# Optimization experiments

Hardware: AMD Instinct MI355X
Metric: run time of the kernel (lower is better)

## Reference

```python
import jax, jax.numpy as jnp
import numpy as np

B, LP, NC, D, E = 8, 1000, 64, 128, 320  # batch, protein len, compound atoms, hid dim, esm dim


def _linear_params(key, din, dout):
    k1, k2 = jax.random.split(key)
    lim = 1.0 / np.sqrt(din)
    W = jax.random.uniform(k1, (din, dout), minval=-lim, maxval=lim, dtype=jnp.float32)
    b = jax.random.uniform(k2, (dout,), minval=-lim, maxval=lim, dtype=jnp.float32)
    return W, b


def setup_inputs() -> dict:
    key = jax.random.key(0)
    ks = jax.random.split(key, 14)
    inp = {
        "protein_embedding": jax.random.normal(ks[0], (B, LP, E), dtype=jnp.float32),
        "protein_feat_x": jax.random.normal(ks[1], (B, LP, D), dtype=jnp.float32),
        "compound_feats": jax.random.normal(ks[2], (B, NC, D), dtype=jnp.float32),
    }
    layers = [("emb", E, D), ("wq", D, D), ("wk", D, D), ("wv", D, D), ("wo", D, D),
              ("jp", D, D), ("jc", D, D),
              ("c1", D, 1024), ("c2", 1024, 1024), ("c3", 1024, 256), ("c4", 256, 1)]
    for i, (name, din, dout) in enumerate(layers):
        W, b = _linear_params(ks[3 + i], din, dout)
        inp[name + "_w"] = W
        inp[name + "_b"] = b
    return inp


def reference(protein_embedding, protein_feat_x, compound_feats,
              emb_w, emb_b, wq_w, wq_b, wk_w, wk_b, wv_w, wv_b, wo_w, wo_b,
              jp_w, jp_b, jc_w, jc_b,
              c1_w, c1_b, c2_w, c2_b, c3_w, c3_b, c4_w, c4_b):
    # protein sequence embedding -> hid dim
    pe = protein_embedding @ emb_w + emb_b                      # [B, LP, D]
    # single-head cross attention: query = seq embedding, key/value = graph feats
    Q = pe @ wq_w + wq_b
    K = protein_feat_x @ wk_w + wk_b
    V = protein_feat_x @ wv_w + wv_b
    scale = jnp.sqrt(jnp.asarray(D, pe.dtype))                  # n_heads=1 -> head_dim=D
    attn = jax.nn.softmax(jnp.einsum('bqd,bkd->bqk', Q, K) / scale, axis=-1)
    protein_feats = jnp.einsum('bqk,bkd->bqd', attn, V) @ wo_w + wo_b  # [B, LP, D]

    # sigmoid bilinear joint attention over (protein residue, compound atom) pairs
    P = jax.nn.relu(protein_feats) @ jp_w + jp_b                # [B, LP, D]
    C = jax.nn.relu(compound_feats) @ jc_w + jc_b               # [B, NC, D]
    A = jax.nn.sigmoid(jnp.einsum('bid,bkd->bik', P, C))        # [B, LP, NC]
    A = A / jnp.sum(A, axis=(1, 2), keepdims=True)

    # tanh outer product (the costly 4D bikj intermediate) then weighted reduction
    cp = jnp.tanh(protein_feats[:, :, None, :] * compound_feats[:, None, :, :])  # [B, LP, NC, D]
    cp_embedding = jnp.einsum('bikd,bik->bd', cp, A)            # [B, D]

    # classifier MLP (dropout is eval-mode identity)
    h = jax.nn.relu(cp_embedding @ c1_w + c1_b)
    h = jax.nn.relu(h @ c2_w + c2_b)
    h = jax.nn.relu(h @ c3_w + c3_b)
    return h @ c4_w + c4_b                                      # [B, 1]
```

## Files before the change

### kernel.cpp

```cpp
#include <hip/hip_runtime.h>
#include <hip/hip_bf16.h>
#include <math.h>

#define LP 1000
#define NCMP 64

__device__ __forceinline__ float rcp_fast(float x) { return __builtin_amdgcn_rcpf(x); }

template<bool RELU_IN>
__device__ __forceinline__ void gemm_body(const float* X, const float* W, const float* __restrict__ bias,
                                          float* Y, int K, int rowbase)
{
    __shared__ __align__(16) float Ws[32][128];
    __shared__ __align__(16) float Xt[32][36];
    const int t  = threadIdx.x;
    const int r0 = (t >> 5) * 4;
    const int c0 = (t & 31) * 4;
    const int xr = t >> 3, xk = (t & 7) << 2;
    const int xrow = rowbase + xr;
    float4 xv = *(const float4*)(X + (long)xrow * K + xk);
    float4 wv[4];
    #pragma unroll
    for (int u = 0; u < 4; ++u) {
        int s = t + u * 256, r = s >> 5, cb = (s & 31) << 2;
        wv[u] = *(const float4*)(W + (long)r * 128 + cb);
    }
    float acc[4][4] = {};
    for (int k0 = 0; k0 < K; k0 += 32) {
        float4 xs = xv;
        if (RELU_IN) { xs.x = fmaxf(xs.x,0.f); xs.y = fmaxf(xs.y,0.f);
                       xs.z = fmaxf(xs.z,0.f); xs.w = fmaxf(xs.w,0.f); }
        Xt[xk+0][xr] = xs.x; Xt[xk+1][xr] = xs.y; Xt[xk+2][xr] = xs.z; Xt[xk+3][xr] = xs.w;
        #pragma unroll
        for (int u = 0; u < 4; ++u) {
            int s = t + u * 256, r = s >> 5, cb = (s & 31) << 2;
            *(float4*)&Ws[r][cb] = wv[u];
        }
        __syncthreads();
        if (k0 + 32 < K) {
            xv = *(const float4*)(X + (long)xrow * K + k0 + 32 + xk);
            #pragma unroll
            for (int u = 0; u < 4; ++u) {
                int s = t + u * 256, r = s >> 5, cb = (s & 31) << 2;
                wv[u] = *(const float4*)(W + (long)(k0 + 32 + r) * 128 + cb);
            }
        }
        #pragma unroll
        for (int kk = 0; kk < 32; ++kk) {
            float4 w4 = *(const float4*)&Ws[kk][c0];
            float4 x4 = *(const float4*)&Xt[kk][r0];
            acc[0][0] = fmaf(x4.x, w4.x, acc[0][0]); acc[0][1] = fmaf(x4.x, w4.y, acc[0][1]);
            acc[0][2] = fmaf(x4.x, w4.z, acc[0][2]); acc[0][3] = fmaf(x4.x, w4.w, acc[0][3]);
            acc[1][0] = fmaf(x4.y, w4.x, acc[1][0]); acc[1][1] = fmaf(x4.y, w4.y, acc[1][1]);
            acc[1][2] = fmaf(x4.y, w4.z, acc[1][2]); acc[1][3] = fmaf(x4.y, w4.w, acc[1][3]);
            acc[2][0] = fmaf(x4.z, w4.x, acc[2][0]); acc[2][1] = fmaf(x4.z, w4.y, acc[2][1]);
            acc[2][2] = fmaf(x4.z, w4.z, acc[2][2]); acc[2][3] = fmaf(x4.z, w4.w, acc[2][3]);
            acc[3][0] = fmaf(x4.w, w4.x, acc[3][0]); acc[3][1] = fmaf(x4.w, w4.y, acc[3][1]);
            acc[3][2] = fmaf(x4.w, w4.z, acc[3][2]); acc[3][3] = fmaf(x4.w, w4.w, acc[3][3]);
        }
        __syncthreads();
    }
    float4 bv = *(const float4*)(bias + c0);
    #pragma unroll
    for (int i = 0; i < 4; ++i) {
        int row = rowbase + r0 + i;
        float4 o;
        o.x = acc[i][0] + bv.x; o.y = acc[i][1] + bv.y;
        o.z = acc[i][2] + bv.z; o.w = acc[i][3] + bv.w;
        *(float4*)(Y + (long)row * 128 + c0) = o;
    }
}

__global__ __launch_bounds__(256) void pre0_k(const float* __restrict__ emb_w, const float* __restrict__ emb_b,
                                              const float* __restrict__ wq_w, const float* __restrict__ wq_b,
                                              const float* __restrict__ wv_w, const float* __restrict__ wv_b,
                                              const float* __restrict__ wo_w, const float* __restrict__ wo_b,
                                              const float* __restrict__ zeros,
                                              float* __restrict__ Wp, float* __restrict__ bp,
                                              float* __restrict__ Wvo, float* __restrict__ bvo)
{
    const int bid = blockIdx.x;
    if (bid < 10) { gemm_body<false>(emb_w, wq_w, zeros, Wp, 128, bid * 32); return; }
    if (bid >= 11 && bid < 15) { gemm_body<false>(wv_w, wo_w, zeros, Wvo, 128, (bid - 11) * 32); return; }
    int n = threadIdx.x;
    if (n < 128) {
        const float* vb = (bid == 10) ? emb_b : wv_b;
        const float* Wm = (bid == 10) ? wq_w  : wo_w;
        const float* ab = (bid == 10) ? wq_b  : wo_b;
        float a0 = 0.f, a1 = 0.f, a2 = 0.f, a3 = 0.f;
        for (int k = 0; k < 128; k += 4) {
            a0 = fmaf(vb[k+0], Wm[(k+0)*128 + n], a0);
            a1 = fmaf(vb[k+1], Wm[(k+1)*128 + n], a1);
            a2 = fmaf(vb[k+2], Wm[(k+2)*128 + n], a2);
            a3 = fmaf(vb[k+3], Wm[(k+3)*128 + n], a3);
        }
        float* dst = (bid == 10) ? bp : bvo;
        dst[n] = (a0 + a1) + (a2 + a3) + ab[n];
    }
}

__global__ __launch_bounds__(256) void qkv_k(const float* __restrict__ PE, const float* __restrict__ Wp,
                                             const float* __restrict__ bp, const float* __restrict__ PFX,
                                             const float* __restrict__ wk_w, const float* __restrict__ wk_b,
                                             const float* __restrict__ CF, const float* __restrict__ jc_w,
                                             const float* __restrict__ jc_b,
                                             float* __restrict__ Qo, float* __restrict__ Ko, float* __restrict__ Cj)
{
    if (blockIdx.x < 250)
        gemm_body<false>(PE, Wp, bp, Qo, 320, blockIdx.x * 32);
    else if (blockIdx.x < 500)
        gemm_body<false>(PFX, wk_w, wk_b, Ko, 128, (blockIdx.x - 250) * 32);
    else
        gemm_body<true>(CF, jc_w, jc_b, Cj, 128, (blockIdx.x - 500) * 32);
}

__global__ __launch_bounds__(256) void flash_k(const float* __restrict__ Q, const float* __restrict__ Kg,
                                               const float* __restrict__ Vg, float* __restrict__ Opart,
                                               float* __restrict__ mpart, float* __restrict__ lpart)
{
    __shared__ __align__(16) float Qs[32][132];
    __shared__ __align__(16) float KVs[64][132];
    __shared__ __align__(16) float Ps[32][68];
    const int t  = threadIdx.x;
    const int tr = t >> 4;
    const int tc = t & 15;
    const int qt = blockIdx.x, sp = blockIdx.y, b = blockIdx.z;
    const int q0 = qt * 32;
    const float SCALE = 0.08838834764831845f;
    const float L2E   = 1.4426950408889634f;

    #pragma unroll
    for (int u = 0; u < 4; ++u) {
        int s = t + u * 256;
        int r = s >> 5, cb = (s & 31) << 2;
        float4 v = make_float4(0.f, 0.f, 0.f, 0.f);
        if (q0 + r < LP) v = *(const float4*)(Q + ((long)b * LP + q0 + r) * 128 + cb);
        Qs[r][cb] = v.x; Qs[r][cb + 1] = v.y; Qs[r][cb + 2] = v.z; Qs[r][cb + 3] = v.w;
    }
    float m_i[2] = { -3.0e38f, -3.0e38f };
    float l_i[2] = { 0.f, 0.f };
    float Oa[2][8] = {};

    for (int kt = sp * 8; kt < sp * 8 + 8; ++kt) {
        const int key0 = kt * 64;
        __syncthreads();
        #pragma unroll
        for (int u = 0; u < 8; ++u) {
            int s = t + u * 256;
            int r = s >> 5, cb = (s & 31) << 2;
            float4 v = make_float4(0.f, 0.f, 0.f, 0.f);
            if (key0 + r < LP) v = *(const float4*)(Kg + ((long)b * LP + key0 + r) * 128 + cb);
            KVs[r][cb] = v.x; KVs[r][cb + 1] = v.y; KVs[r][cb + 2] = v.z; KVs[r][cb + 3] = v.w;
        }
        __syncthreads();
        float sacc[2][4] = {};
        #pragma unroll 4
        for (int d4 = 0; d4 < 32; ++d4) {
            float4 q0v = *(const float4*)&Qs[2 * tr][d4 << 2];
            float4 q1v = *(const float4*)&Qs[2 * tr + 1][d4 << 2];
            #pragma unroll
            for (int j = 0; j < 4; ++j) {
                float4 kv = *(const float4*)&KVs[tc + (j << 4)][d4 << 2];
                sacc[0][j] += q0v.x * kv.x + q0v.y * kv.y + q0v.z * kv.z + q0v.w * kv.w;
                sacc[1][j] += q1v.x * kv.x + q1v.y * kv.y + q1v.z * kv.z + q1v.w * kv.w;
            }
        }
        __syncthreads();
        float4 vreg[8];
        #pragma unroll
        for (int u = 0; u < 8; ++u) {
            int s = t + u * 256;
            int r = s >> 5, cb = (s & 31) << 2;
            float4 v = make_float4(0.f, 0.f, 0.f, 0.f);
            if (key0 + r < LP) v = *(const float4*)(Vg + ((long)b * LP + key0 + r) * 128 + cb);
            vreg[u] = v;
        }
        #pragma unroll
        for (int j = 0; j < 4; ++j) {
            bool valid = (key0 + tc + (j << 4)) < LP;
            #pragma unroll
            for (int i = 0; i < 2; ++i) {
                float sv = sacc[i][j] * SCALE;
                sacc[i][j] = valid ? sv : -3.0e38f;
            }
        }
        #pragma unroll
        for (int i = 0; i < 2; ++i) {
            float tm = fmaxf(fmaxf(sacc[i][0], sacc[i][1]), fmaxf(sacc[i][2], sacc[i][3]));
            tm = fmaxf(tm, __shfl_xor(tm, 1));
            tm = fmaxf(tm, __shfl_xor(tm, 2));
            tm = fmaxf(tm, __shfl_xor(tm, 4));
            tm = fmaxf(tm, __shfl_xor(tm, 8));
            float mnew  = fmaxf(m_i[i], tm);
            float alpha = exp2f((m_i[i] - mnew) * L2E);
            float ps = 0.f;
            #pragma unroll
            for (int j = 0; j < 4; ++j) {
                float p = exp2f((sacc[i][j] - mnew) * L2E);
                Ps[2 * tr + i][tc + (j << 4)] = p;
                ps += p;
            }
            ps += __shfl_xor(ps, 1);
            ps += __shfl_xor(ps, 2);
            ps += __shfl_xor(ps, 4);
            ps += __shfl_xor(ps, 8);
            l_i[i] = l_i[i] * alpha + ps;
            m_i[i] = mnew;
            #pragma unroll
            for (int j = 0; j < 8; ++j) Oa[i][j] *= alpha;
        }
        #pragma unroll
        for (int u = 0; u < 8; ++u) {
            int s = t + u * 256;
            int r = s >> 5, cb = (s & 31) << 2;
            KVs[r][cb] = vreg[u].x; KVs[r][cb + 1] = vreg[u].y;
            KVs[r][cb + 2] = vreg[u].z; KVs[r][cb + 3] = vreg[u].w;
        }
        __syncthreads();
        #pragma unroll 2
        for (int c = 0; c < 64; ++c) {
            float4 va = *(const float4*)&KVs[c][tc << 2];
            float4 vb = *(const float4*)&KVs[c][64 + (tc << 2)];
            float p0 = Ps[2 * tr][c];
            float p1 = Ps[2 * tr + 1][c];
            Oa[0][0] = fmaf(p0, va.x, Oa[0][0]); Oa[0][1] = fmaf(p0, va.y, Oa[0][1]);
            Oa[0][2] = fmaf(p0, va.z, Oa[0][2]); Oa[0][3] = fmaf(p0, va.w, Oa[0][3]);
            Oa[0][4] = fmaf(p0, vb.x, Oa[0][4]); Oa[0][5] = fmaf(p0, vb.y, Oa[0][5]);
            Oa[0][6] = fmaf(p0, vb.z, Oa[0][6]); Oa[0][7] = fmaf(p0, vb.w, Oa[0][7]);
            Oa[1][0] = fmaf(p1, va.x, Oa[1][0]); Oa[1][1] = fmaf(p1, va.y, Oa[1][1]);
            Oa[1][2] = fmaf(p1, va.z, Oa[1][2]); Oa[1][3] = fmaf(p1, va.w, Oa[1][3]);
            Oa[1][4] = fmaf(p1, vb.x, Oa[1][4]); Oa[1][5] = fmaf(p1, vb.y, Oa[1][5]);
            Oa[1][6] = fmaf(p1, vb.z, Oa[1][6]); Oa[1][7] = fmaf(p1, vb.w, Oa[1][7]);
        }
    }
    #pragma unroll
    for (int i = 0; i < 2; ++i) {
        int row = q0 + 2 * tr + i;
        if (row < LP) {
            long base = (((long)sp * 8 + b) * LP + row) * 128;
            *(float4*)(Opart + base + (tc << 2))      = make_float4(Oa[i][0], Oa[i][1], Oa[i][2], Oa[i][3]);
            *(float4*)(Opart + base + 64 + (tc << 2)) = make_float4(Oa[i][4], Oa[i][5], Oa[i][6], Oa[i][7]);
            if (tc == 0) {
                mpart[((long)sp * 8 + b) * LP + row] = m_i[i];
                lpart[((long)sp * 8 + b) * LP + row] = l_i[i];
            }
        }
    }
}

__global__ __launch_bounds__(256) void megatail_k(
    const float* __restrict__ Opart, const float* __restrict__ mp, const float* __restrict__ lp,
    const float* __restrict__ Wvo, const float* __restrict__ bvo,
    const float* __restrict__ jp_w, const float* __restrict__ jp_b,
    const float* __restrict__ Cj, const float* __restrict__ CF,
    float* __restrict__ Asum, float* __restrict__ cpe)
{
    __shared__ __align__(16) float WsA[32][132];
    __shared__ __align__(16) float Xt[32][20];
    __shared__ __align__(16) float AttS[16][132];
    __shared__ __align__(16) float Csh[64][132];
    __shared__ float Ash[16][64];
    __shared__ float red[256];
    const int t = threadIdx.x;
    const int p0 = blockIdx.x * 16;
    const int b  = blockIdx.y;
    const float L2E = 1.4426950408889634f;

    #pragma unroll
    for (int u = 0; u < 8; ++u) {
        int s = t + u * 256, r = s >> 5, cb = (s & 31) << 2;
        float4 v = *(const float4*)(Cj + ((long)b * NCMP + r) * 128 + cb);
        Csh[r][cb] = v.x; Csh[r][cb+1] = v.y; Csh[r][cb+2] = v.z; Csh[r][cb+3] = v.w;
    }

    const int r0 = (t >> 5) * 2, c0 = (t & 31) * 4;
    const int xr = t >> 3, xk = (t & 7) << 2;
    int prow = p0 + xr; if (prow > LP - 1) prow = LP - 1;
    const long g = (long)b * LP + prow;
    float w0 = 0.f, w1 = 0.f, linv = 0.f;
    if (t < 128) {
        float m0 = mp[g], m1 = mp[g + 8000];
        float l0 = lp[g], l1 = lp[g + 8000];
        float mm = fmaxf(m0, m1);
        w0 = exp2f((m0 - mm) * L2E); w1 = exp2f((m1 - mm) * L2E);
        linv = 1.0f / (w0 * l0 + w1 * l1);
    }
    float4 xv = make_float4(0.f,0.f,0.f,0.f);
    float4 wv[4];
    if (t < 128) {
        float4 a = *(const float4*)(Opart + g * 128 + xk);
        float4 c = *(const float4*)(Opart + 1024000 + g * 128 + xk);
        xv.x = (w0*a.x + w1*c.x) * linv; xv.y = (w0*a.y + w1*c.y) * linv;
        xv.z = (w0*a.z + w1*c.z) * linv; xv.w = (w0*a.w + w1*c.w) * linv;
    }
    #pragma unroll
    for (int u = 0; u < 4; ++u) {
        int s = t + u * 256, r = s >> 5, cb = (s & 31) << 2;
        wv[u] = *(const float4*)(Wvo + (long)r * 128 + cb);
    }
    float acc[2][4] = {};
    for (int k0 = 0; k0 < 128; k0 += 32) {
        if (t < 128) { Xt[xk+0][xr]=xv.x; Xt[xk+1][xr]=xv.y; Xt[xk+2][xr]=xv.z; Xt[xk+3][xr]=xv.w; }
        #pragma unroll
        for (int u = 0; u < 4; ++u) {
            int s = t + u * 256, r = s >> 5, cb = (s & 31) << 2;
            *(float4*)&WsA[r][cb] = wv[u];
        }
        __syncthreads();
        if (k0 + 32 < 128) {
            int kn = k0 + 32;
            if (t < 128) {
                float4 a = *(const float4*)(Opart + g * 128 + kn + xk);
                float4 c = *(const float4*)(Opart + 1024000 + g * 128 + kn + xk);
                xv.x = (w0*a.x + w1*c.x) * linv; xv.y = (w0*a.y + w1*c.y) * linv;
                xv.z = (w0*a.z + w1*c.z) * linv; xv.w = (w0*a.w + w1*c.w) * linv;
            }
            #pragma unroll
            for (int u = 0; u < 4; ++u) {
                int s = t + u * 256, r = s >> 5, cb = (s & 31) << 2;
                wv[u] = *(const float4*)(Wvo + (long)(kn + r) * 128 + cb);
            }
        }
        #pragma unroll
        for (int kk = 0; kk < 32; ++kk) {
            float2 x2 = *(const float2*)&Xt[kk][r0];
            float4 w4 = *(const float4*)&WsA[kk][c0];
            acc[0][0]=fmaf(x2.x,w4.x,acc[0][0]); acc[0][1]=fmaf(x2.x,w4.y,acc[0][1]);
            acc[0][2]=fmaf(x2.x,w4.z,acc[0][2]); acc[0][3]=fmaf(x2.x,w4.w,acc[0][3]);
            acc[1][0]=fmaf(x2.y,w4.x,acc[1][0]); acc[1][1]=fmaf(x2.y,w4.y,acc[1][1]);
            acc[1][2]=fmaf(x2.y,w4.z,acc[1][2]); acc[1][3]=fmaf(x2.y,w4.w,acc[1][3]);
        }
        __syncthreads();
    }
    {
        float4 bv1 = *(const float4*)(bvo + c0);
        #pragma unroll
        for (int i = 0; i < 2; ++i) {
            float4 o = make_float4(acc[i][0]+bv1.x, acc[i][1]+bv1.y, acc[i][2]+bv1.z, acc[i][3]+bv1.w);
            *(float4*)&AttS[r0 + i][c0] = o;
        }
    }
    float4 wv2[4];
    #pragma unroll
    for (int u = 0; u < 4; ++u) {
        int s = t + u * 256, r = s >> 5, cb = (s & 31) << 2;
        wv2[u] = *(const float4*)(jp_w + (long)r * 128 + cb);
    }
    float ac2[2][4] = {};
    for (int k0 = 0; k0 < 128; k0 += 32) {
        #pragma unroll
        for (int u = 0; u < 4; ++u) {
            int s = t + u * 256, r = s >> 5, cb = (s & 31) << 2;
            *(float4*)&WsA[r][cb] = wv2[u];
        }
        __syncthreads();
        if (k0 + 32 < 128) {
            #pragma unroll
            for (int u = 0; u < 4; ++u) {
                int s = t + u * 256, r = s >> 5, cb = (s & 31) << 2;
                wv2[u] = *(const float4*)(jp_w + (long)(k0 + 32 + r) * 128 + cb);
            }
        }
        #pragma unroll
        for (int kk = 0; kk < 32; ++kk) {
            float x0 = fmaxf(AttS[r0 + 0][k0 + kk], 0.f);
            float x1 = fmaxf(AttS[r0 + 1][k0 + kk], 0.f);
            float4 w4 = *(const float4*)&WsA[kk][c0];
            ac2[0][0]=fmaf(x0,w4.x,ac2[0][0]); ac2[0][1]=fmaf(x0,w4.y,ac2[0][1]);
            ac2[0][2]=fmaf(x0,w4.z,ac2[0][2]); ac2[0][3]=fmaf(x0,w4.w,ac2[0][3]);
            ac2[1][0]=fmaf(x1,w4.x,ac2[1][0]); ac2[1][1]=fmaf(x1,w4.y,ac2[1][1]);
            ac2[1][2]=fmaf(x1,w4.z,ac2[1][2]); ac2[1][3]=fmaf(x1,w4.w,ac2[1][3]);
        }
        __syncthreads();
    }
    float (*Psh)[132] = WsA;
    {
        float4 b2 = *(const float4*)(jp_b + c0);
        #pragma unroll
        for (int i = 0; i < 2; ++i)
            *(float4*)&Psh[r0 + i][c0] =
                make_float4(ac2[i][0]+b2.x, ac2[i][1]+b2.y, ac2[i][2]+b2.z, ac2[i][3]+b2.w);
    }
    __syncthreads();
    const int tr = t >> 4, tc = t & 15;
    float sacc[4] = {};
    #pragma unroll 4
    for (int d4 = 0; d4 < 32; ++d4) {
        float4 p4 = *(const float4*)&Psh[tr][d4 << 2];
        #pragma unroll
        for (int j = 0; j < 4; ++j) {
            float4 cv = *(const float4*)&Csh[tc + (j << 4)][d4 << 2];
            sacc[j] += p4.x*cv.x + p4.y*cv.y + p4.z*cv.z + p4.w*cv.w;
        }
    }
    float lsum = 0.f;
    {
        int gi = p0 + tr;
        #pragma unroll
        for (int j = 0; j < 4; ++j) {
            float sg = rcp_fast(1.f + exp2f(-sacc[j] * L2E));
            if (gi < LP) { Ash[tr][tc + (j << 4)] = sg; lsum += sg; }
        }
    }
    red[t] = lsum;
    __syncthreads();
    for (int off = 128; off > 0; off >>= 1) {
        if (t < off) red[t] += red[t + off];
        __syncthreads();
    }
    if (t == 0) atomicAdd(Asum + b, red[0]);
    __syncthreads();
    #pragma unroll
    for (int u = 0; u < 8; ++u) {
        int s = t + u * 256, r = s >> 5, cb = (s & 31) << 2;
        float4 v = *(const float4*)(CF + ((long)b * NCMP + r) * 128 + cb);
        Csh[r][cb] = v.x; Csh[r][cb+1] = v.y; Csh[r][cb+2] = v.z; Csh[r][cb+3] = v.w;
    }
    __syncthreads();
    const float TWO_L2E = 2.8853900817779268f;
    const int d  = t & 127;
    const int kh = t >> 7;
    const int iiN = (LP - p0 < 16) ? (LP - p0) : 16;
    float accD = 0.f;
    for (int ii = 0; ii < iiN; ++ii) {
        float ptl = AttS[ii][d] * TWO_L2E;
        #pragma unroll
        for (int kk = 0; kk < 32; ++kk) {
            int k = (kh << 5) + kk;
            float e  = exp2f(ptl * Csh[k][d]);
            float th = 1.f - 2.f * rcp_fast(e + 1.f);
            accD = fmaf(th, Ash[ii][k], accD);
        }
    }
    red[t] = accD;
    __syncthreads();
    if (t < 128) atomicAdd(cpe + (long)b * 128 + t, red[t] + red[t + 128]);
}

__global__ __launch_bounds__(256) void c1h_k(const float* __restrict__ cpe, const float* __restrict__ Asum,
                                             const float* __restrict__ W, const float* __restrict__ bias,
                                             float* __restrict__ h1)
{
    __shared__ float sc[8][128];
    const int t = threadIdx.x;
    #pragma unroll
    for (int u = 0; u < 4; ++u) {
        int idx = t + u * 256;
        sc[idx >> 7][idx & 127] = cpe[idx] * rcp_fast(Asum[idx >> 7]);
    }
    __syncthreads();
    const int b = t >> 5, n = blockIdx.x * 32 + (t & 31);
    float a0 = 0.f, a1 = 0.f, a2 = 0.f, a3 = 0.f;
    #pragma unroll 8
    for (int k = 0; k < 128; k += 4) {
        a0 = fmaf(sc[b][k+0], W[(long)(k+0)*1024 + n], a0);
        a1 = fmaf(sc[b][k+1], W[(long)(k+1)*1024 + n], a1);
        a2 = fmaf(sc[b][k+2], W[(long)(k+2)*1024 + n], a2);
        a3 = fmaf(sc[b][k+3], W[(long)(k+3)*1024 + n], a3);
    }
    h1[b * 1024 + n] = fmaxf((a0 + a1) + (a2 + a3) + bias[n], 0.f);
}

__global__ __launch_bounds__(256) void c2_part_k(const float* __restrict__ in, const float* __restrict__ W,
                                                 float* __restrict__ part)
{
    __shared__ float ins[8][16];
    const int t = threadIdx.x, ks = blockIdx.x, k0 = ks * 16;
    if (t < 128) {
        int b = t >> 4, kk = t & 15;
        ins[b][kk] = in[b * 1024 + k0 + kk];
    }
    __syncthreads();
    const int n = (t & 63) * 4 + (t >> 6) * 256;
    float4 acc[8] = {};
    #pragma unroll
    for (int kk = 0; kk < 16; ++kk) {
        float4 w4 = *(const float4*)(W + (long)(k0 + kk) * 1024 + n);
        #pragma unroll
        for (int b = 0; b < 8; ++b) {
            float s = ins[b][kk];
            acc[b].x = fmaf(s, w4.x, acc[b].x); acc[b].y = fmaf(s, w4.y, acc[b].y);
            acc[b].z = fmaf(s, w4.z, acc[b].z); acc[b].w = fmaf(s, w4.w, acc[b].w);
        }
    }
    #pragma unroll
    for (int b = 0; b < 8; ++b)
        *(float4*)(part + ((long)(ks * 8 + b)) * 1024 + n) = acc[b];
}

__global__ __launch_bounds__(256) void c3m_k(const float* __restrict__ part2, const float* __restrict__ c2_b,
                                             const float* __restrict__ c3_w, const float* __restrict__ c3_b,
                                             const float* __restrict__ c4_w, const float* __restrict__ c4_b,
                                             float* __restrict__ out)
{
    __shared__ float Hs[1024];
    __shared__ float red[256];
    const int t = threadIdx.x, b = blockIdx.x;
    float4 acc4 = make_float4(0.f,0.f,0.f,0.f);
    #pragma unroll 4
    for (int ks = 0; ks < 64; ++ks) {
        float4 p = *(const float4*)(part2 + ((long)(ks * 8 + b)) * 1024 + t * 4);
        acc4.x += p.x; acc4.y += p.y; acc4.z += p.z; acc4.w += p.w;
    }
    {
        float4 bb = *(const float4*)(c2_b + t * 4);
        Hs[t*4+0] = fmaxf(acc4.x + bb.x, 0.f);
        Hs[t*4+1] = fmaxf(acc4.y + bb.y, 0.f);
        Hs[t*4+2] = fmaxf(acc4.z + bb.z, 0.f);
        Hs[t*4+3] = fmaxf(acc4.w + bb.w, 0.f);
    }
    __syncthreads();
    float a0 = 0.f, a1 = 0.f, a2 = 0.f, a3 = 0.f;
    #pragma unroll 8
    for (int k = 0; k < 1024; k += 4) {
        a0 = fmaf(Hs[k+0], c3_w[(long)(k+0)*256 + t], a0);
        a1 = fmaf(Hs[k+1], c3_w[(long)(k+1)*256 + t], a1);
        a2 = fmaf(Hs[k+2], c3_w[(long)(k+2)*256 + t], a2);
        a3 = fmaf(Hs[k+3], c3_w[(long)(k+3)*256 + t], a3);
    }
    float h3v = fmaxf((a0 + a1) + (a2 + a3) + c3_b[t], 0.f);
    red[t] = h3v * c4_w[t];
    __syncthreads();
    for (int off = 128; off > 0; off >>= 1) {
        if (t < off) red[t] += red[t + off];
        __syncthreads();
    }
    if (t == 0) out[b] = red[0] + c4_b[0];
}

extern "C" void kernel_launch(void* const* d_in, const int* in_sizes, int n_in,
                              void* d_out, int out_size, void* d_ws, size_t ws_size,
                              hipStream_t stream)
{
    const float* PE   = (const float*)d_in[0];
    const float* PFX  = (const float*)d_in[1];
    const float* CF   = (const float*)d_in[2];
    const float* emb_w = (const float*)d_in[3];  const float* emb_b = (const float*)d_in[4];
    const float* wq_w  = (const float*)d_in[5];  const float* wq_b  = (const float*)d_in[6];
    const float* wk_w  = (const float*)d_in[7];  const float* wk_b  = (const float*)d_in[8];
    const float* wv_w  = (const float*)d_in[9];  const float* wv_b  = (const float*)d_in[10];
    const float* wo_w  = (const float*)d_in[11]; const float* wo_b  = (const float*)d_in[12];
    const float* jp_w  = (const float*)d_in[13]; const float* jp_b  = (const float*)d_in[14];
    const float* jc_w  = (const float*)d_in[15]; const float* jc_b  = (const float*)d_in[16];
    const float* c1_w  = (const float*)d_in[17]; const float* c1_b  = (const float*)d_in[18];
    const float* c2_w  = (const float*)d_in[19]; const float* c2_b  = (const float*)d_in[20];
    const float* c3_w  = (const float*)d_in[21]; const float* c3_b  = (const float*)d_in[22];
    const float* c4_w  = (const float*)d_in[23]; const float* c4_b  = (const float*)d_in[24];

    float* ws     = (float*)d_ws;
    float* bufQ   = ws;
    float* bufK   = bufQ   + 1024000;
    float* bufC   = bufK   + 1024000;
    float* Opart  = bufC   + 65536;
    float* mpart  = Opart  + 2048000;
    float* lpart  = mpart  + 16000;
    float* Asum   = lpart  + 16000;
    float* cpe    = Asum   + 8;
    float* zeros  = cpe    + 1024;
    float* bprime = zeros  + 128;
    float* bufWp  = bprime + 128;
    float* bufWvo = bufWp  + 40960;
    float* bufbvo = bufWvo + 16384;
    float* h1     = bufbvo + 128;
    float* part2  = bufQ;

    hipMemsetAsync(Asum, 0, (8 + 1024 + 128) * sizeof(float), stream);

    pre0_k<<<16, 256, 0, stream>>>(emb_w, emb_b, wq_w, wq_b, wv_w, wv_b, wo_w, wo_b,
                                   zeros, bufWp, bprime, bufWvo, bufbvo);
    qkv_k<<<516, 256, 0, stream>>>(PE, bufWp, bprime, PFX, wk_w, wk_b, CF, jc_w, jc_b,
                                   bufQ, bufK, bufC);
    flash_k<<<dim3(32, 2, 8), 256, 0, stream>>>(bufQ, bufK, PFX, Opart, mpart, lpart);
    megatail_k<<<dim3(63, 8), 256, 0, stream>>>(Opart, mpart, lpart, bufWvo, bufbvo,
                                                jp_w, jp_b, bufC, CF, Asum, cpe);
    c1h_k<<<32, 256, 0, stream>>>(cpe, Asum, c1_w, c1_b, h1);
    c2_part_k<<<64, 256, 0, stream>>>(h1, c2_w, part2);
    c3m_k<<<8, 256, 0, stream>>>(part2, c2_b, c3_w, c3_b, c4_w, c4_b, (float*)d_out);
}
```

Before: 336.4 us.

## Retile flash attention to 48-row tiles with three-way key split; fuse c1 into c2

The flash attention kernel now gives each thread three query rows instead of two (48-row tiles) and splits the key range three ways instead of two, giving 504 blocks instead of 512 with more register reuse of each K/V load. The P·V loop reads probabilities as float4. The merge in the tail kernel is generalized to NSPLIT partials. The c1 layer is fused into the c2 partial kernel, which removes a launch and the h1 buffer. In exchange, each c12 block recomputes a small c1 slice, and register pressure in the attention kernel goes up.

```diff
diff --git a/kernel.cpp b/kernel.cpp
--- a/kernel.cpp
+++ b/kernel.cpp
@@ -4,6 +4,7 @@
 
 #define LP 1000
 #define NCMP 64
+#define NSPLIT 3
 
 __device__ __forceinline__ float rcp_fast(float x) { return __builtin_amdgcn_rcpf(x); }
 
@@ -114,78 +115,78 @@
         gemm_body<true>(CF, jc_w, jc_b, Cj, 128, (blockIdx.x - 500) * 32);
 }
 
-__global__ __launch_bounds__(256) void flash_k(const float* __restrict__ Q, const float* __restrict__ Kg,
-                                               const float* __restrict__ Vg, float* __restrict__ Opart,
-                                               float* __restrict__ mpart, float* __restrict__ lpart)
-{
-    __shared__ __align__(16) float Qs[32][132];
+__global__ __launch_bounds__(256) void flash6_k(const float* __restrict__ Q, const float* __restrict__ Kg,
+                                                const float* __restrict__ Vg, float* __restrict__ Opart,
+                                                float* __restrict__ mpart, float* __restrict__ lpart)
+{
+    __shared__ __align__(16) float Qs[48][132];
     __shared__ __align__(16) float KVs[64][132];
-    __shared__ __align__(16) float Ps[32][68];
+    __shared__ __align__(16) float Ps[48][68];
     const int t  = threadIdx.x;
     const int tr = t >> 4;
     const int tc = t & 15;
     const int qt = blockIdx.x, sp = blockIdx.y, b = blockIdx.z;
-    const int q0 = qt * 32;
+    const int q0 = qt * 48;
+    const int kt0 = (sp * 16) / NSPLIT;
+    const int kt1 = ((sp + 1) * 16) / NSPLIT;
     const float SCALE = 0.08838834764831845f;
     const float L2E   = 1.4426950408889634f;
 
     #pragma unroll
-    for (int u = 0; u < 4; ++u) {
-        int s = t + u * 256;
-        int r = s >> 5, cb = (s & 31) << 2;
+    for (int u = 0; u < 6; ++u) {
+        int s = t + u * 256, r = s >> 5, cb = (s & 31) << 2;
         float4 v = make_float4(0.f, 0.f, 0.f, 0.f);
         if (q0 + r < LP) v = *(const float4*)(Q + ((long)b * LP + q0 + r) * 128 + cb);
-        Qs[r][cb] = v.x; Qs[r][cb + 1] = v.y; Qs[r][cb + 2] = v.z; Qs[r][cb + 3] = v.w;
-    }
-    float m_i[2] = { -3.0e38f, -3.0e38f };
-    float l_i[2] = { 0.f, 0.f };
-    float Oa[2][8] = {};
-
-    for (int kt = sp * 8; kt < sp * 8 + 8; ++kt) {
+        *(float4*)&Qs[r][cb] = v;
+    }
+    float m_i[3] = { -3.0e38f, -3.0e38f, -3.0e38f };
+    float l_i[3] = { 0.f, 0.f, 0.f };
+    float Oa[3][8] = {};
+
+    for (int kt = kt0; kt < kt1; ++kt) {
         const int key0 = kt * 64;
         __syncthreads();
         #pragma unroll
         for (int u = 0; u < 8; ++u) {
-            int s = t + u * 256;
-            int r = s >> 5, cb = (s & 31) << 2;
+            int s = t + u * 256, r = s >> 5, cb = (s & 31) << 2;
             float4 v = make_float4(0.f, 0.f, 0.f, 0.f);
             if (key0 + r < LP) v = *(const float4*)(Kg + ((long)b * LP + key0 + r) * 128 + cb);
-            KVs[r][cb] = v.x; KVs[r][cb + 1] = v.y; KVs[r][cb + 2] = v.z; KVs[r][cb + 3] = v.w;
-        }
-        __syncthreads();
-        float sacc[2][4] = {};
+            *(float4*)&KVs[r][cb] = v;
+        }
+        __syncthreads();
+        float sacc[3][4] = {};
         #pragma unroll 4
         for (int d4 = 0; d4 < 32; ++d4) {
-            float4 q0v = *(const float4*)&Qs[2 * tr][d4 << 2];
-            float4 q1v = *(const float4*)&Qs[2 * tr + 1][d4 << 2];
+            float4 q0v = *(const float4*)&Qs[3 * tr + 0][d4 << 2];
+            float4 q1v = *(const float4*)&Qs[3 * tr + 1][d4 << 2];
+            float4 q2v = *(const float4*)&Qs[3 * tr + 2][d4 << 2];
             #pragma unroll
             for (int j = 0; j < 4; ++j) {
                 float4 kv = *(const float4*)&KVs[tc + (j << 4)][d4 << 2];
-                sacc[0][j] += q0v.x * kv.x + q0v.y * kv.y + q0v.z * kv.z + q0v.w * kv.w;
-                sacc[1][j] += q1v.x * kv.x + q1v.y * kv.y + q1v.z * kv.z + q1v.w * kv.w;
+                sacc[0][j] += q0v.x*kv.x + q0v.y*kv.y + q0v.z*kv.z + q0v.w*kv.w;
+                sacc[1][j] += q1v.x*kv.x + q1v.y*kv.y + q1v.z*kv.z + q1v.w*kv.w;
+                sacc[2][j] += q2v.x*kv.x + q2v.y*kv.y + q2v.z*kv.z + q2v.w*kv.w;
             }
         }
         __syncthreads();
         float4 vreg[8];
         #pragma unroll
         for (int u = 0; u < 8; ++u) {
-            int s = t + u * 256;
-            int r = s >> 5, cb = (s & 31) << 2;
-            float4 v = make_float4(0.f, 0.f, 0.f, 0.f);
-            if (key0 + r < LP) v = *(const float4*)(Vg + ((long)b * LP + key0 + r) * 128 + cb);
-            vreg[u] = v;
+            int s = t + u * 256, r = s >> 5, cb = (s & 31) << 2;
+            vreg[u] = make_float4(0.f, 0.f, 0.f, 0.f);
+            if (key0 + r < LP) vreg[u] = *(const float4*)(Vg + ((long)b * LP + key0 + r) * 128 + cb);
         }
         #pragma unroll
         for (int j = 0; j < 4; ++j) {
             bool valid = (key0 + tc + (j << 4)) < LP;
             #pragma unroll
-            for (int i = 0; i < 2; ++i) {
+            for (int i = 0; i < 3; ++i) {
                 float sv = sacc[i][j] * SCALE;
                 sacc[i][j] = valid ? sv : -3.0e38f;
             }
         }
         #pragma unroll
-        for (int i = 0; i < 2; ++i) {
+        for (int i = 0; i < 3; ++i) {
             float tm = fmaxf(fmaxf(sacc[i][0], sacc[i][1]), fmaxf(sacc[i][2], sacc[i][3]));
             tm = fmaxf(tm, __shfl_xor(tm, 1));
             tm = fmaxf(tm, __shfl_xor(tm, 2));
@@ -197,7 +198,7 @@
             #pragma unroll
             for (int j = 0; j < 4; ++j) {
                 float p = exp2f((sacc[i][j] - mnew) * L2E);
-                Ps[2 * tr + i][tc + (j << 4)] = p;
+                Ps[3 * tr + i][tc + (j << 4)] = p;
                 ps += p;
             }
             ps += __shfl_xor(ps, 1);
@@ -211,38 +212,48 @@
         }
         #pragma unroll
         for (int u = 0; u < 8; ++u) {
-            int s = t + u * 256;
-            int r = s >> 5, cb = (s & 31) << 2;
-            KVs[r][cb] = vreg[u].x; KVs[r][cb + 1] = vreg[u].y;
-            KVs[r][cb + 2] = vreg[u].z; KVs[r][cb + 3] = vreg[u].w;
+            int s = t + u * 256, r = s >> 5, cb = (s & 31) << 2;
+            *(float4*)&KVs[r][cb] = vreg[u];
         }
         __syncthreads();
         #pragma unroll 2
-        for (int c = 0; c < 64; ++c) {
-            float4 va = *(const float4*)&KVs[c][tc << 2];
-            float4 vb = *(const float4*)&KVs[c][64 + (tc << 2)];
-            float p0 = Ps[2 * tr][c];
-            float p1 = Ps[2 * tr + 1][c];
-            Oa[0][0] = fmaf(p0, va.x, Oa[0][0]); Oa[0][1] = fmaf(p0, va.y, Oa[0][1]);
-            Oa[0][2] = fmaf(p0, va.z, Oa[0][2]); Oa[0][3] = fmaf(p0, va.w, Oa[0][3]);
-            Oa[0][4] = fmaf(p0, vb.x, Oa[0][4]); Oa[0][5] = fmaf(p0, vb.y, Oa[0][5]);
-            Oa[0][6] = fmaf(p0, vb.z, Oa[0][6]); Oa[0][7] = fmaf(p0, vb.w, Oa[0][7]);
-            Oa[1][0] = fmaf(p1, va.x, Oa[1][0]); Oa[1][1] = fmaf(p1, va.y, Oa[1][1]);
-            Oa[1][2] = fmaf(p1, va.z, Oa[1][2]); Oa[1][3] = fmaf(p1, va.w, Oa[1][3]);
-            Oa[1][4] = fmaf(p1, vb.x, Oa[1][4]); Oa[1][5] = fmaf(p1, vb.y, Oa[1][5]);
-            Oa[1][6] = fmaf(p1, vb.z, Oa[1][6]); Oa[1][7] = fmaf(p1, vb.w, Oa[1][7]);
-        }
-    }
-    #pragma unroll
-    for (int i = 0; i < 2; ++i) {
-        int row = q0 + 2 * tr + i;
+        for (int cg = 0; cg < 16; ++cg) {
+            float4 pa = *(const float4*)&Ps[3 * tr + 0][cg << 2];
+            float4 pb = *(const float4*)&Ps[3 * tr + 1][cg << 2];
+            float4 pc = *(const float4*)&Ps[3 * tr + 2][cg << 2];
+            #pragma unroll
+            for (int e = 0; e < 4; ++e) {
+                int c = (cg << 2) + e;
+                float4 va = *(const float4*)&KVs[c][tc << 2];
+                float4 vb = *(const float4*)&KVs[c][64 + (tc << 2)];
+                float p0 = (e == 0) ? pa.x : (e == 1) ? pa.y : (e == 2) ? pa.z : pa.w;
+                float p1 = (e == 0) ? pb.x : (e == 1) ? pb.y : (e == 2) ? pb.z : pb.w;
+                float p2 = (e == 0) ? pc.x : (e == 1) ? pc.y : (e == 2) ? pc.z : pc.w;
+                Oa[0][0] = fmaf(p0, va.x, Oa[0][0]); Oa[0][1] = fmaf(p0, va.y, Oa[0][1]);
+                Oa[0][2] = fmaf(p0, va.z, Oa[0][2]); Oa[0][3] = fmaf(p0, va.w, Oa[0][3]);
+                Oa[0][4] = fmaf(p0, vb.x, Oa[0][4]); Oa[0][5] = fmaf(p0, vb.y, Oa[0][5]);
+                Oa[0][6] = fmaf(p0, vb.z, Oa[0][6]); Oa[0][7] = fmaf(p0, vb.w, Oa[0][7]);
+                Oa[1][0] = fmaf(p1, va.x, Oa[1][0]); Oa[1][1] = fmaf(p1, va.y, Oa[1][1]);
+                Oa[1][2] = fmaf(p1, va.z, Oa[1][2]); Oa[1][3] = fmaf(p1, va.w, Oa[1][3]);
+                Oa[1][4] = fmaf(p1, vb.x, Oa[1][4]); Oa[1][5] = fmaf(p1, vb.y, Oa[1][5]);
+                Oa[1][6] = fmaf(p1, vb.z, Oa[1][6]); Oa[1][7] = fmaf(p1, vb.w, Oa[1][7]);
+                Oa[2][0] = fmaf(p2, va.x, Oa[2][0]); Oa[2][1] = fmaf(p2, va.y, Oa[2][1]);
+                Oa[2][2] = fmaf(p2, va.z, Oa[2][2]); Oa[2][3] = fmaf(p2, va.w, Oa[2][3]);
+                Oa[2][4] = fmaf(p2, vb.x, Oa[2][4]); Oa[2][5] = fmaf(p2, vb.y, Oa[2][5]);
+                Oa[2][6] = fmaf(p2, vb.z, Oa[2][6]); Oa[2][7] = fmaf(p2, vb.w, Oa[2][7]);
+            }
+        }
+    }
+    #pragma unroll
+    for (int i = 0; i < 3; ++i) {
+        int row = q0 + 3 * tr + i;
         if (row < LP) {
-            long base = (((long)sp * 8 + b) * LP + row) * 128;
+            long base = ((long)sp * 1024000) + ((long)b * LP + row) * 128;
             *(float4*)(Opart + base + (tc << 2))      = make_float4(Oa[i][0], Oa[i][1], Oa[i][2], Oa[i][3]);
             *(float4*)(Opart + base + 64 + (tc << 2)) = make_float4(Oa[i][4], Oa[i][5], Oa[i][6], Oa[i][7]);
             if (tc == 0) {
-                mpart[((long)sp * 8 + b) * LP + row] = m_i[i];
-                lpart[((long)sp * 8 + b) * LP + row] = l_i[i];
+                mpart[(long)sp * 8000 + b * LP + row] = m_i[i];
+                lpart[(long)sp * 8000 + b * LP + row] = l_i[i];
             }
         }
     }
@@ -269,29 +280,37 @@
     #pragma unroll
     for (int u = 0; u < 8; ++u) {
         int s = t + u * 256, r = s >> 5, cb = (s & 31) << 2;
-        float4 v = *(const float4*)(Cj + ((long)b * NCMP + r) * 128 + cb);
-        Csh[r][cb] = v.x; Csh[r][cb+1] = v.y; Csh[r][cb+2] = v.z; Csh[r][cb+3] = v.w;
+        *(float4*)&Csh[r][cb] = *(const float4*)(Cj + ((long)b * NCMP + r) * 128 + cb);
     }
 
     const int r0 = (t >> 5) * 2, c0 = (t & 31) * 4;
     const int xr = t >> 3, xk = (t & 7) << 2;
     int prow = p0 + xr; if (prow > LP - 1) prow = LP - 1;
     const long g = (long)b * LP + prow;
-    float w0 = 0.f, w1 = 0.f, linv = 0.f;
+    float wgt[NSPLIT]; float linv = 0.f;
     if (t < 128) {
-        float m0 = mp[g], m1 = mp[g + 8000];
-        float l0 = lp[g], l1 = lp[g + 8000];
-        float mm = fmaxf(m0, m1);
-        w0 = exp2f((m0 - mm) * L2E); w1 = exp2f((m1 - mm) * L2E);
-        linv = 1.0f / (w0 * l0 + w1 * l1);
+        float mm = -3.0e38f;
+        #pragma unroll
+        for (int s = 0; s < NSPLIT; ++s) mm = fmaxf(mm, mp[g + (long)s * 8000]);
+        float ls = 0.f;
+        #pragma unroll
+        for (int s = 0; s < NSPLIT; ++s) {
+            wgt[s] = exp2f((mp[g + (long)s * 8000] - mm) * L2E);
+            ls += wgt[s] * lp[g + (long)s * 8000];
+        }
+        linv = 1.0f / ls;
     }
     float4 xv = make_float4(0.f,0.f,0.f,0.f);
     float4 wv[4];
     if (t < 128) {
-        float4 a = *(const float4*)(Opart + g * 128 + xk);
-        float4 c = *(const float4*)(Opart + 1024000 + g * 128 + xk);
-        xv.x = (w0*a.x + w1*c.x) * linv; xv.y = (w0*a.y + w1*c.y) * linv;
-        xv.z = (w0*a.z + w1*c.z) * linv; xv.w = (w0*a.w + w1*c.w) * linv;
+        float4 a = make_float4(0.f,0.f,0.f,0.f);
+        #pragma unroll
+        for (int s = 0; s < NSPLIT; ++s) {
+            float4 p = *(const float4*)(Opart + (long)s * 1024000 + g * 128 + xk);
+            a.x = fmaf(wgt[s], p.x, a.x); a.y = fmaf(wgt[s], p.y, a.y);
+            a.z = fmaf(wgt[s], p.z, a.z); a.w = fmaf(wgt[s], p.w, a.w);
+        }
+        xv = make_float4(a.x * linv, a.y * linv, a.z * linv, a.w * linv);
     }
     #pragma unroll
     for (int u = 0; u < 4; ++u) {
@@ -310,10 +329,14 @@
         if (k0 + 32 < 128) {
             int kn = k0 + 32;
             if (t < 128) {
-                float4 a = *(const float4*)(Opart + g * 128 + kn + xk);
-                float4 c = *(const float4*)(Opart + 1024000 + g * 128 + kn + xk);
-                xv.x = (w0*a.x + w1*c.x) * linv; xv.y = (w0*a.y + w1*c.y) * linv;
-                xv.z = (w0*a.z + w1*c.z) * linv; xv.w = (w0*a.w + w1*c.w) * linv;
+                float4 a = make_float4(0.f,0.f,0.f,0.f);
+                #pragma unroll
+                for (int s = 0; s < NSPLIT; ++s) {
+                    float4 p = *(const float4*)(Opart + (long)s * 1024000 + g * 128 + kn + xk);
+                    a.x = fmaf(wgt[s], p.x, a.x); a.y = fmaf(wgt[s], p.y, a.y);
+                    a.z = fmaf(wgt[s], p.z, a.z); a.w = fmaf(wgt[s], p.w, a.w);
+                }
+                xv = make_float4(a.x * linv, a.y * linv, a.z * linv, a.w * linv);
             }
             #pragma unroll
             for (int u = 0; u < 4; ++u) {
@@ -335,10 +358,9 @@
     {
         float4 bv1 = *(const float4*)(bvo + c0);
         #pragma unroll
-        for (int i = 0; i < 2; ++i) {
-            float4 o = make_float4(acc[i][0]+bv1.x, acc[i][1]+bv1.y, acc[i][2]+bv1.z, acc[i][3]+bv1.w);
-            *(float4*)&AttS[r0 + i][c0] = o;
-        }
+        for (int i = 0; i < 2; ++i)
+            *(float4*)&AttS[r0 + i][c0] =
+                make_float4(acc[i][0]+bv1.x, acc[i][1]+bv1.y, acc[i][2]+bv1.z, acc[i][3]+bv1.w);
     }
     float4 wv2[4];
     #pragma unroll
@@ -413,8 +435,7 @@
     #pragma unroll
     for (int u = 0; u < 8; ++u) {
         int s = t + u * 256, r = s >> 5, cb = (s & 31) << 2;
-        float4 v = *(const float4*)(CF + ((long)b * NCMP + r) * 128 + cb);
-        Csh[r][cb] = v.x; Csh[r][cb+1] = v.y; Csh[r][cb+2] = v.z; Csh[r][cb+3] = v.w;
+        *(float4*)&Csh[r][cb] = *(const float4*)(CF + ((long)b * NCMP + r) * 128 + cb);
     }
     __syncthreads();
     const float TWO_L2E = 2.8853900817779268f;
@@ -437,45 +458,38 @@
     if (t < 128) atomicAdd(cpe + (long)b * 128 + t, red[t] + red[t + 128]);
 }
 
-__global__ __launch_bounds__(256) void c1h_k(const float* __restrict__ cpe, const float* __restrict__ Asum,
-                                             const float* __restrict__ W, const float* __restrict__ bias,
-                                             float* __restrict__ h1)
+__global__ __launch_bounds__(256) void c12_k(const float* __restrict__ cpe, const float* __restrict__ Asum,
+                                             const float* __restrict__ c1_w, const float* __restrict__ c1_b,
+                                             const float* __restrict__ c2_w, float* __restrict__ part)
 {
     __shared__ float sc[8][128];
-    const int t = threadIdx.x;
+    __shared__ float ins[8][16];
+    const int t = threadIdx.x, ks = blockIdx.x, k0 = ks * 16;
     #pragma unroll
     for (int u = 0; u < 4; ++u) {
         int idx = t + u * 256;
         sc[idx >> 7][idx & 127] = cpe[idx] * rcp_fast(Asum[idx >> 7]);
     }
     __syncthreads();
-    const int b = t >> 5, n = blockIdx.x * 32 + (t & 31);
-    float a0 = 0.f, a1 = 0.f, a2 = 0.f, a3 = 0.f;
-    #pragma unroll 8
-    for (int k = 0; k < 128; k += 4) {
-        a0 = fmaf(sc[b][k+0], W[(long)(k+0)*1024 + n], a0);
-        a1 = fmaf(sc[b][k+1], W[(long)(k+1)*1024 + n], a1);
-        a2 = fmaf(sc[b][k+2], W[(long)(k+2)*1024 + n], a2);
-        a3 = fmaf(sc[b][k+3], W[(long)(k+3)*1024 + n], a3);
-    }
-    h1[b * 1024 + n] = fmaxf((a0 + a1) + (a2 + a3) + bias[n], 0.f);
-}
-
-__global__ __launch_bounds__(256) void c2_part_k(const float* __restrict__ in, const float* __restrict__ W,
-                                                 float* __restrict__ part)
-{
-    __shared__ float ins[8][16];
-    const int t = threadIdx.x, ks = blockIdx.x, k0 = ks * 16;
     if (t < 128) {
         int b = t >> 4, kk = t & 15;
-        ins[b][kk] = in[b * 1024 + k0 + kk];
+        int n1 = k0 + kk;
+        float a0 = 0.f, a1 = 0.f, a2 = 0.f, a3 = 0.f;
+        #pragma unroll 8
+        for (int j = 0; j < 128; j += 4) {
+            a0 = fmaf(sc[b][j+0], c1_w[(long)(j+0)*1024 + n1], a0);
+            a1 = fmaf(sc[b][j+1], c1_w[(long)(j+1)*1024 + n1], a1);
+            a2 = fmaf(sc[b][j+2], c1_w[(long)(j+2)*1024 + n1], a2);
+            a3 = fmaf(sc[b][j+3], c1_w[(long)(j+3)*1024 + n1], a3);
+        }
+        ins[b][kk] = fmaxf((a0 + a1) + (a2 + a3) + c1_b[n1], 0.f);
     }
     __syncthreads();
     const int n = (t & 63) * 4 + (t >> 6) * 256;
     float4 acc[8] = {};
     #pragma unroll
     for (int kk = 0; kk < 16; ++kk) {
-        float4 w4 = *(const float4*)(W + (long)(k0 + kk) * 1024 + n);
+        float4 w4 = *(const float4*)(c2_w + (long)(k0 + kk) * 1024 + n);
         #pragma unroll
         for (int b = 0; b < 8; ++b) {
             float s = ins[b][kk];
@@ -552,16 +566,15 @@
     float* bufK   = bufQ   + 1024000;
     float* bufC   = bufK   + 1024000;
     float* Opart  = bufC   + 65536;
-    float* mpart  = Opart  + 2048000;
-    float* lpart  = mpart  + 16000;
-    float* Asum   = lpart  + 16000;
+    float* mpart  = Opart  + 3072000;
+    float* lpart  = mpart  + 24000;
+    float* Asum   = lpart  + 24000;
     float* cpe    = Asum   + 8;
     float* zeros  = cpe    + 1024;
     float* bprime = zeros  + 128;
     float* bufWp  = bprime + 128;
     float* bufWvo = bufWp  + 40960;
     float* bufbvo = bufWvo + 16384;
-    float* h1     = bufbvo + 128;
     float* part2  = bufQ;
 
     hipMemsetAsync(Asum, 0, (8 + 1024 + 128) * sizeof(float), stream);
@@ -570,10 +583,9 @@
                                    zeros, bufWp, bprime, bufWvo, bufbvo);
     qkv_k<<<516, 256, 0, stream>>>(PE, bufWp, bprime, PFX, wk_w, wk_b, CF, jc_w, jc_b,
                                    bufQ, bufK, bufC);
-    flash_k<<<dim3(32, 2, 8), 256, 0, stream>>>(bufQ, bufK, PFX, Opart, mpart, lpart);
+    flash6_k<<<dim3(21, NSPLIT, 8), 256, 0, stream>>>(bufQ, bufK, PFX, Opart, mpart, lpart);
     megatail_k<<<dim3(63, 8), 256, 0, stream>>>(Opart, mpart, lpart, bufWvo, bufbvo,
                                                 jp_w, jp_b, bufC, CF, Asum, cpe);
-    c1h_k<<<32, 256, 0, stream>>>(cpe, Asum, c1_w, c1_b, h1);
-    c2_part_k<<<64, 256, 0, stream>>>(h1, c2_w, part2);
+    c12_k<<<64, 256, 0, stream>>>(cpe, Asum, c1_w, c1_b, c2_w, part2);
     c3m_k<<<8, 256, 0, stream>>>(part2, c2_b, c3_w, c3_b, c4_w, c4_b, (float*)d_out);
 }
```

Result: no change. 336.5 us (+0.0%).
